# Kernel tuning notes

Measured on AMD Instinct MI355X. Metric: run time of the kernel, lower is better.

Reference implementation:

```python
import jax, jax.numpy as jnp
import numpy as np

GAMMA = 0.99

def _get_D(gamma, T, dtype=jnp.float32):
    # D[n, m] = gamma**(n-m) if n >= m else 0 (NaN/inf cleanup as in torch source)
    n = jnp.arange(T)
    diff = n[:, None] - n[None, :]
    return jnp.where(diff >= 0, jnp.power(jnp.asarray(gamma, dtype), jnp.maximum(diff, 0).astype(dtype)), jnp.zeros((), dtype))

def setup_inputs() -> dict:
    key = jax.random.key(0)
    kX, kQ, kK, kV = jax.random.split(key, 4)
    B, T, I, C = 2, 4096, 1024, 1024
    X = jax.random.normal(kX, (B, T, I), dtype=jnp.float32)
    att_mask = jnp.ones((B, T), dtype=jnp.float32)
    S_n = jnp.zeros((B, C, C), dtype=jnp.float32)
    # params initialized as randn/I per the torch module
    W_Q = jax.random.normal(kQ, (I, C), dtype=jnp.float32) / I
    W_K = jax.random.normal(kK, (I, C), dtype=jnp.float32) / I
    W_V = jax.random.normal(kV, (I, I), dtype=jnp.float32) / I
    return {"X": X, "att_mask": att_mask, "S_n": S_n, "W_Q": W_Q, "W_K": W_K, "W_V": W_V}

def reference(X, att_mask, S_n, W_Q, W_K, W_V):
    # COINBlock.forward_parallel (dropout in eval mode = identity; att_mask unused)
    B, T, _ = X.shape
    C = W_Q.shape[1]
    Q = X @ W_Q            # [B,T,C]
    K = X @ W_K            # [B,T,C]
    V = X @ W_V            # [B,T,I]
    A = jnp.einsum('btc,bsc->bts', Q, K)          # [B,T,T]
    A = A * _get_D(GAMMA, T, X.dtype)[None, :, :]  # decay-masked scores
    out = A @ V                                    # [B,T,I]
    out = jnp.swapaxes(out, -2, -1).reshape(B, T, C)  # faithful transpose+view (I == C)
    return out, S_n
```

## Files before the change

kernel.cpp:

```cpp
#include <hip/hip_runtime.h>
#include <cstdint>
#include <cstddef>


using bf16x8 = __attribute__((ext_vector_type(8))) short;
using s16x4  = __attribute__((ext_vector_type(4))) short;
using f32x4  = __attribute__((ext_vector_type(4))) float;

#define T_SEQ 4096
#define C_DIM 1024

static constexpr float L2G = -0.0144995697f;

__device__ __forceinline__ short f2bf(float f) {
  unsigned u = __builtin_bit_cast(unsigned, f);
  u += 0x7FFFu + ((u >> 16) & 1u);
  return (short)(u >> 16);
}

__device__ __forceinline__ void async_ld16(const short* g, const short* l) {
  __builtin_amdgcn_global_load_lds(
      (const __attribute__((address_space(1))) unsigned int*)(uintptr_t)g,
      (__attribute__((address_space(3))) unsigned int*)(unsigned)(uintptr_t)l,
      16, 0, 0);
}

#define FENCE asm volatile("" ::: "memory")
#define BAR   do { FENCE; __builtin_amdgcn_s_barrier(); FENCE; } while (0)
#define VMC(N) asm volatile("s_waitcnt vmcnt(" #N ")" ::: "memory")


__device__ __forceinline__ void gemm4p2(
    const short* __restrict__ A, const short* __restrict__ B,
    int lda, int ldb, int NT,
    short* __restrict__ lsA, short* __restrict__ lsB,
    f32x4 (&acc)[4][4])
{
  const int tid  = threadIdx.x;
  const int lane = tid & 63;
  const int wave = tid >> 6;
  const int wM   = wave >> 1;
  const int wN   = wave & 1;
  const int quad = lane >> 4;
  const int l15  = lane & 15;
  const int key  = l15 & 7;
  const int uk0  = (quad ^ key) * 8;
  const int uk1  = ((4 ^ quad) ^ key) * 8;
  const short* aR0 = lsA + (wM * 64 + l15) * 64 + uk0;
  const short* aR1 = lsA + (wM * 64 + l15) * 64 + uk1;
  const short* bR0 = lsB + (wN * 64 + l15) * 64 + uk0;
  const short* bR1 = lsB + (wN * 64 + l15) * 64 + uk1;
  const int rl0 = lane >> 3;
  const int cu  = ((lane & 7) ^ rl0) * 8;
  const short* pa[2][2];
  const short* pb[2][2];
#pragma unroll
  for (int u = 0; u < 2; ++u)
#pragma unroll
    for (int j = 0; j < 2; ++j) {
      pa[u][j] = A + (size_t)(u * 64 + (wave + 4 * j) * 8 + rl0) * lda + cu;
      pb[u][j] = B + (size_t)(u * 64 + (wave + 4 * j) * 8 + rl0) * ldb + cu;
    }

#define S4A(SLOT, TT)                                                               \
  { _Pragma("unroll")                                                               \
    for (int u = 0; u < 2; ++u)                                                     \
      _Pragma("unroll")                                                             \
      for (int j = 0; j < 2; ++j)                                                   \
        async_ld16(pa[u][j] + (size_t)(TT) * 64,                                    \
                   lsA + (SLOT) * 8192 + u * 4096 + (wave + 4 * j) * 512 + lane * 8); }
#define S4B(SLOT, TT)                                                               \
  { _Pragma("unroll")                                                               \
    for (int u = 0; u < 2; ++u)                                                     \
      _Pragma("unroll")                                                             \
      for (int j = 0; j < 2; ++j)                                                   \
        async_ld16(pb[u][j] + (size_t)(TT) * 64,                                    \
                   lsB + (SLOT) * 8192 + u * 4096 + (wave + 4 * j) * 512 + lane * 8); }

  bf16x8 afA[4][2], afB[4][2], b01A[2][2], b01B[2][2], b23[2][2];

#define RD_AF(DST, SLOT)                                                            \
  { _Pragma("unroll")                                                               \
    for (int i = 0; i < 4; ++i) {                                                   \
      DST[i][0] = *(const bf16x8*)(aR0 + (SLOT) * 8192 + i * 1024);                 \
      DST[i][1] = *(const bf16x8*)(aR1 + (SLOT) * 8192 + i * 1024);                 \
    } }
#define RD_B01(DST, SLOT)                                                           \
  { _Pragma("unroll")                                                               \
    for (int n = 0; n < 2; ++n) {                                                   \
      DST[n][0] = *(const bf16x8*)(bR0 + (SLOT) * 8192 + n * 1024);                 \
      DST[n][1] = *(const bf16x8*)(bR1 + (SLOT) * 8192 + n * 1024);                 \
    } }
#define RD_B23(SLOT)                                                                \
  { _Pragma("unroll")                                                               \
    for (int n = 0; n < 2; ++n) {                                                   \
      b23[n][0] = *(const bf16x8*)(bR0 + (SLOT) * 8192 + (2 + n) * 1024);           \
      b23[n][1] = *(const bf16x8*)(bR1 + (SLOT) * 8192 + (2 + n) * 1024);           \
    } }
#define MFLO(AF, B01)                                                               \
  { __builtin_amdgcn_s_setprio(1);                                                  \
    _Pragma("unroll")                                                               \
    for (int kk = 0; kk < 2; ++kk)                                                  \
      _Pragma("unroll")                                                             \
      for (int i = 0; i < 4; ++i)                                                   \
        _Pragma("unroll")                                                           \
        for (int n = 0; n < 2; ++n)                                                 \
          acc[i][n] = __builtin_amdgcn_mfma_f32_16x16x32_bf16(                      \
              AF[i][kk], B01[n][kk], acc[i][n], 0, 0, 0);                           \
    __builtin_amdgcn_s_setprio(0); }
#define MFHI(AF)                                                                    \
  { __builtin_amdgcn_s_setprio(1);                                                  \
    _Pragma("unroll")                                                               \
    for (int kk = 0; kk < 2; ++kk)                                                  \
      _Pragma("unroll")                                                             \
      for (int i = 0; i < 4; ++i)                                                   \
        _Pragma("unroll")                                                           \
        for (int n = 0; n < 2; ++n)                                                 \
          acc[i][2 + n] = __builtin_amdgcn_mfma_f32_16x16x32_bf16(                  \
              AF[i][kk], b23[n][kk], acc[i][2 + n], 0, 0, 0);                       \
    __builtin_amdgcn_s_setprio(0); }

  S4A(0, 0); S4B(0, 0); S4A(1, 1); S4B(1, 1);
  VMC(8);
  BAR;
  RD_AF(afA, 0);
  RD_B01(b01A, 0);

  int s0 = 0;
  for (int tp = 0; tp < NT; tp += 2) {
    int s1 = s0 + 1; if (s1 == 3) s1 = 0;
    int s2 = s1 + 1; if (s2 == 3) s2 = 0;
    const int s3 = s0;
    const bool g2 = (tp + 2 < NT);
    const bool g3 = (tp + 3 < NT);

    RD_B23(s0);
    if (g2) S4B(s2, tp + 2);
    MFLO(afA, b01A);
    if (g2) VMC(4); else VMC(0);
    BAR;
    RD_AF(afB, 1);
    RD_B01(b01B, s1);
    if (g2) S4A(0, tp + 2);
    MFHI(afA);
    if (g2) VMC(4); else VMC(0);
    BAR;
    RD_B23(s1);
    if (g3) S4B(s3, tp + 3);
    MFLO(afB, b01B);
    if (g3) VMC(4); else VMC(0);
    BAR;
    if (g2) { RD_AF(afA, 0); RD_B01(b01A, s2); }
    if (g3) S4A(1, tp + 3);
    MFHI(afB);
    if (g3) VMC(4); else VMC(0);
    BAR;

    s0 = s2;
  }
#undef S4A
#undef S4B
#undef RD_AF
#undef RD_B01
#undef RD_B23
#undef MFLO
#undef MFHI
}

__device__ __forceinline__ void gemm4p3(
    const short* __restrict__ A, const short* __restrict__ B,
    int lda, int ldb, int NT,
    short* __restrict__ lsA, short* __restrict__ lsB,
    f32x4 (&acc)[4][4])
{
  const int tid  = threadIdx.x;
  const int lane = tid & 63;
  const int wave = tid >> 6;
  const int wM   = wave >> 1;
  const int wN   = wave & 1;
  const int quad = lane >> 4;
  const int l15  = lane & 15;
  const int key  = l15 & 7;
  const int uk0  = (quad ^ key) * 8;
  const int uk1  = ((4 ^ quad) ^ key) * 8;
  const short* aR0 = lsA + (wM * 64 + l15) * 64 + uk0;
  const short* aR1 = lsA + (wM * 64 + l15) * 64 + uk1;
  const short* bR0 = lsB + (wN * 64 + l15) * 64 + uk0;
  const short* bR1 = lsB + (wN * 64 + l15) * 64 + uk1;
  const int rl0 = lane >> 3;
  const int cu  = ((lane & 7) ^ rl0) * 8;
  const short* pa[2][2];
  const short* pb[2][2];
#pragma unroll
  for (int u = 0; u < 2; ++u)
#pragma unroll
    for (int j = 0; j < 2; ++j) {
      pa[u][j] = A + (size_t)(u * 64 + (wave + 4 * j) * 8 + rl0) * lda + cu;
      pb[u][j] = B + (size_t)(u * 64 + (wave + 4 * j) * 8 + rl0) * ldb + cu;
    }

#define S4A(SLOT, TT)                                                               \
  { _Pragma("unroll")                                                               \
    for (int u = 0; u < 2; ++u)                                                     \
      _Pragma("unroll")                                                             \
      for (int j = 0; j < 2; ++j)                                                   \
        async_ld16(pa[u][j] + (size_t)(TT) * 64,                                    \
                   lsA + (SLOT) * 8192 + u * 4096 + (wave + 4 * j) * 512 + lane * 8); }
#define S4B(SLOT, TT)                                                               \
  { _Pragma("unroll")                                                               \
    for (int u = 0; u < 2; ++u)                                                     \
      _Pragma("unroll")                                                             \
      for (int j = 0; j < 2; ++j)                                                   \
        async_ld16(pb[u][j] + (size_t)(TT) * 64,                                    \
                   lsB + (SLOT) * 8192 + u * 4096 + (wave + 4 * j) * 512 + lane * 8); }

  bf16x8 afA[4][2], afB[4][2], b01A[2][2], b01B[2][2], b23[2][2];

#define RD_AF(DST, SLOT)                                                            \
  { _Pragma("unroll")                                                               \
    for (int i = 0; i < 4; ++i) {                                                   \
      DST[i][0] = *(const bf16x8*)(aR0 + (SLOT) * 8192 + i * 1024);                 \
      DST[i][1] = *(const bf16x8*)(aR1 + (SLOT) * 8192 + i * 1024);                 \
    } }
#define RD_B01(DST, SLOT)                                                           \
  { _Pragma("unroll")                                                               \
    for (int n = 0; n < 2; ++n) {                                                   \
      DST[n][0] = *(const bf16x8*)(bR0 + (SLOT) * 8192 + n * 1024);                 \
      DST[n][1] = *(const bf16x8*)(bR1 + (SLOT) * 8192 + n * 1024);                 \
    } }
#define RD_B23(SLOT)                                                                \
  { _Pragma("unroll")                                                               \
    for (int n = 0; n < 2; ++n) {                                                   \
      b23[n][0] = *(const bf16x8*)(bR0 + (SLOT) * 8192 + (2 + n) * 1024);           \
      b23[n][1] = *(const bf16x8*)(bR1 + (SLOT) * 8192 + (2 + n) * 1024);           \
    } }
#define MFLO(AF, B01)                                                               \
  { __builtin_amdgcn_s_setprio(1);                                                  \
    _Pragma("unroll")                                                               \
    for (int kk = 0; kk < 2; ++kk)                                                  \
      _Pragma("unroll")                                                             \
      for (int i = 0; i < 4; ++i)                                                   \
        _Pragma("unroll")                                                           \
        for (int n = 0; n < 2; ++n)                                                 \
          acc[i][n] = __builtin_amdgcn_mfma_f32_16x16x32_bf16(                      \
              AF[i][kk], B01[n][kk], acc[i][n], 0, 0, 0);                           \
    __builtin_amdgcn_s_setprio(0); }
#define MFHI(AF)                                                                    \
  { __builtin_amdgcn_s_setprio(1);                                                  \
    _Pragma("unroll")                                                               \
    for (int kk = 0; kk < 2; ++kk)                                                  \
      _Pragma("unroll")                                                             \
      for (int i = 0; i < 4; ++i)                                                   \
        _Pragma("unroll")                                                           \
        for (int n = 0; n < 2; ++n)                                                 \
          acc[i][2 + n] = __builtin_amdgcn_mfma_f32_16x16x32_bf16(                  \
              AF[i][kk], b23[n][kk], acc[i][2 + n], 0, 0, 0);                       \
    __builtin_amdgcn_s_setprio(0); }

  S4A(0, 0); S4B(0, 0); S4A(1, 1); S4B(1, 1);
  VMC(8);
  BAR;
  RD_AF(afA, 0);
  RD_B01(b01A, 0);

  int s0 = 0;
  for (int tp = 0; tp < NT; tp += 2) {
    int s1 = s0 + 1; if (s1 == 3) s1 = 0;
    int s2 = s1 + 1; if (s2 == 3) s2 = 0;
    const int s3 = s0;
    const bool g2 = (tp + 2 < NT);
    const bool g3 = (tp + 3 < NT);

    RD_B23(s0);
    if (g2) S4A(s2, tp + 2);
    MFLO(afA, b01A);
    if (g2) VMC(4); else VMC(0);
    BAR;
    RD_AF(afB, s1);
    RD_B01(b01B, s1);
    if (g2) S4B(s2, tp + 2);
    MFHI(afA);
    if (g2) VMC(4); else VMC(0);
    BAR;
    RD_B23(s1);
    if (g3) S4A(s3, tp + 3);
    MFLO(afB, b01B);
    if (g3) VMC(4); else VMC(0);
    BAR;
    if (g2) { RD_AF(afA, s2); RD_B01(b01A, s2); }
    if (g3) S4B(s3, tp + 3);
    MFHI(afB);
    if (g3) VMC(4); else VMC(0);
    BAR;

    s0 = s2;
  }
#undef S4A
#undef S4B
#undef RD_AF
#undef RD_B01
#undef RD_B23
#undef MFLO
#undef MFHI
}


__global__ __launch_bounds__(256) void k_convX(const float* __restrict__ x,
                                               short* __restrict__ y) {
  const size_t i = ((size_t)blockIdx.x * 256 + threadIdx.x) * 4;
  const float4 v = *(const float4*)(x + i);
  s16x4 o;
  o[0] = f2bf(v.x); o[1] = f2bf(v.y); o[2] = f2bf(v.z); o[3] = f2bf(v.w);
  *(s16x4*)(y + i) = o;
}

__global__ __launch_bounds__(256) void k_convWt(const float* __restrict__ Wq,
                                                const float* __restrict__ Wk,
                                                const float* __restrict__ Wv,
                                                short* __restrict__ Wtq,
                                                short* __restrict__ Wtk,
                                                short* __restrict__ Wtv) {
  const float* W = (blockIdx.z == 0) ? Wq : (blockIdx.z == 1) ? Wk : Wv;
  short* Wt      = (blockIdx.z == 0) ? Wtq : (blockIdx.z == 1) ? Wtk : Wtv;
  __shared__ float t[32][33];
  const int tx = threadIdx.x & 31;
  const int ty = threadIdx.x >> 5;
  const int bc = blockIdx.x * 32;
  const int bi = blockIdx.y * 32;
#pragma unroll
  for (int j = 0; j < 32; j += 8)
    t[ty + j][tx] = W[(size_t)(bi + ty + j) * 1024 + bc + tx];
  __syncthreads();
#pragma unroll
  for (int j = 0; j < 32; j += 8)
    Wt[(size_t)(bc + ty + j) * 1024 + bi + tx] = f2bf(t[tx][ty + j]);
}


__global__ __launch_bounds__(256, 2) void k_proj(
    const short* __restrict__ Xb, const short* __restrict__ Wtq,
    const short* __restrict__ Wtk, const short* __restrict__ Wtv,
    short* __restrict__ Qb, short* __restrict__ Kb, short* __restrict__ Vt) {
  __shared__ short lsA[2 * 8192];
  __shared__ short lsB[3 * 8192];
  f32x4 acc[4][4];
#pragma unroll
  for (int i = 0; i < 4; ++i)
#pragma unroll
    for (int j = 0; j < 4; ++j) acc[i][j] = 0.f;

  const int z  = blockIdx.y;
  const int bx = blockIdx.x;
  const short* Ab;
  const short* Bb;
  int m, n;
  if (z < 2) {
    m = bx >> 3; n = bx & 7;
    Ab = Xb + (size_t)m * 128 * 1024;
    Bb = (z ? Wtk : Wtq) + (size_t)n * 128 * 1024;
  } else {
    m = bx >> 6; n = bx & 63;
    Ab = Wtv + (size_t)m * 128 * 1024;
    Bb = Xb + (size_t)n * 128 * 1024;
  }
  gemm4p2(Ab, Bb, 1024, 1024, 16, lsA, lsB, acc);

  const int lane = threadIdx.x & 63, wave = threadIdx.x >> 6;
  const int wM = wave >> 1, wN = wave & 1;
  const int quad = lane >> 4, l15 = lane & 15;
  if (z < 2) {
    short* O = z ? Kb : Qb;
#pragma unroll
    for (int mi = 0; mi < 4; ++mi)
#pragma unroll
      for (int ni = 0; ni < 4; ++ni)
#pragma unroll
        for (int r = 0; r < 4; ++r) {
          const int row = m * 128 + wM * 64 + mi * 16 + quad * 4 + r;
          const int col = n * 128 + wN * 64 + ni * 16 + l15;
          O[(size_t)row * 1024 + col] = f2bf(acc[mi][ni][r]);
        }
  } else {
#pragma unroll
    for (int mi = 0; mi < 4; ++mi)
#pragma unroll
      for (int ni = 0; ni < 4; ++ni)
#pragma unroll
        for (int r = 0; r < 4; ++r) {
          const int crow = m * 128 + wM * 64 + mi * 16 + quad * 4 + r;
          const int t8   = n * 128 + wN * 64 + ni * 16 + l15;
          const int b = t8 >> 12, tt = t8 & 4095;
          Vt[(size_t)b * C_DIM * T_SEQ + (size_t)crow * T_SEQ + tt] =
              f2bf(acc[mi][ni][r]);
        }
  }
}

__global__ __launch_bounds__(256, 2) void k_scores(const short* __restrict__ Qb,
                                                   const short* __restrict__ Kb,
                                                   short* __restrict__ P) {
  __shared__ short lsA[2 * 8192];
  __shared__ short lsB[3 * 8192];
  f32x4 acc[4][4];
#pragma unroll
  for (int i = 0; i < 4; ++i)
#pragma unroll
    for (int j = 0; j < 4; ++j) acc[i][j] = 0.f;

  int id = blockIdx.x, mm = 0;
  while (id >= 32 - mm) { id -= 32 - mm; ++mm; }
  const int nn = mm + id;

  const size_t b = blockIdx.y;
  const short* Ab = Qb + b * T_SEQ * C_DIM + (size_t)nn * 128 * 1024;
  const short* Bb = Kb + b * T_SEQ * C_DIM + (size_t)mm * 128 * 1024;
  gemm4p2(Ab, Bb, 1024, 1024, 16, lsA, lsB, acc);

  short* Pb = P + b * (size_t)T_SEQ * T_SEQ;
  const int lane = threadIdx.x & 63, wave = threadIdx.x >> 6;
  const int wM = wave >> 1, wN = wave & 1;
  const int quad = lane >> 4, l15 = lane & 15;
#pragma unroll
  for (int mi = 0; mi < 4; ++mi)
#pragma unroll
    for (int ni = 0; ni < 4; ++ni)
#pragma unroll
      for (int r = 0; r < 4; ++r) {
        const int n = nn * 128 + wM * 64 + mi * 16 + quad * 4 + r;
        const int m = mm * 128 + wN * 64 + ni * 16 + l15;
        float v = 0.f;
        if (n >= m) v = acc[mi][ni][r] * exp2f((float)(n - m) * L2G);
        Pb[(size_t)n * T_SEQ + m] = f2bf(v);
      }
}

__global__ __launch_bounds__(256, 1) void k_pv(const short* __restrict__ Vt,
                                               const short* __restrict__ P,
                                               float* __restrict__ out) {
  __shared__ short lsA[3 * 8192];
  __shared__ short lsB[3 * 8192];
  const int p  = blockIdx.x;
  const int iy = blockIdx.y;
  const size_t b = blockIdx.z;

  const short* Ab = Vt + b * (size_t)C_DIM * T_SEQ + (size_t)iy * 128 * T_SEQ;
  const short* Pb = P + b * (size_t)T_SEQ * T_SEQ;
  float* Ob = out + b * (size_t)C_DIM * T_SEQ;

  const int lane = threadIdx.x & 63, wave = threadIdx.x >> 6;
  const int wM = wave >> 1, wN = wave & 1;
  const int quad = lane >> 4, l15 = lane & 15;

  const int cols[2] = { 31 - p, p };
#pragma unroll
  for (int cc = 0; cc < 2; ++cc) {
    const int c = cols[cc];
    f32x4 acc[4][4];
#pragma unroll
    for (int i = 0; i < 4; ++i)
#pragma unroll
      for (int j = 0; j < 4; ++j) acc[i][j] = 0.f;
    gemm4p3(Ab, Pb + (size_t)c * 128 * T_SEQ, T_SEQ, T_SEQ, 2 * c + 2,
            lsA, lsB, acc);
#pragma unroll
    for (int mi = 0; mi < 4; ++mi)
#pragma unroll
      for (int ni = 0; ni < 4; ++ni)
#pragma unroll
        for (int r = 0; r < 4; ++r) {
          const int irow = iy * 128 + wM * 64 + mi * 16 + quad * 4 + r;
          const int tcol = c * 128 + wN * 64 + ni * 16 + l15;
          Ob[(size_t)irow * T_SEQ + tcol] = acc[mi][ni][r];
        }
  }
}


extern "C" void kernel_launch(void* const* d_in, const int* in_sizes, int n_in,
                              void* d_out, int out_size, void* d_ws, size_t ws_size,
                              hipStream_t stream) {
  const float* X  = (const float*)d_in[0];
  const float* Wq = (const float*)d_in[3];
  const float* Wk = (const float*)d_in[4];
  const float* Wv = (const float*)d_in[5];
  float* out = (float*)d_out;

  char* ws = (char*)d_ws;
  short* Xb  = (short*)(ws);
  short* Wtq = (short*)(ws + 16777216);
  short* Wtk = (short*)(ws + 18874368);
  short* Wtv = (short*)(ws + 20971520);
  short* Qb  = (short*)(ws + 23068672);
  short* Kb  = (short*)(ws + 39845888);
  short* Vt  = (short*)(ws + 56623104);
  short* P   = (short*)(ws + 73400320);

  const size_t mainN = (size_t)2 * T_SEQ * C_DIM;
  hipMemsetAsync((char*)d_out + mainN * 4, 0,
                 ((size_t)out_size - mainN) * 4, stream);

  k_convX  <<<dim3(8192),       dim3(256), 0, stream>>>(X, Xb);
  k_convWt <<<dim3(32, 32, 3),  dim3(256), 0, stream>>>(Wq, Wk, Wv, Wtq, Wtk, Wtv);
  k_proj   <<<dim3(512, 3),     dim3(256), 0, stream>>>(Xb, Wtq, Wtk, Wtv, Qb, Kb, Vt);
  k_scores <<<dim3(528, 2),     dim3(256), 0, stream>>>(Qb, Kb, P);
  k_pv     <<<dim3(16, 8, 2),   dim3(256), 0, stream>>>(Vt, P, out);
}
```

Before: 269.3 us.

## Use 256x256 tiles with 8-wave GEMM for scores and remap blocks across XCDs

Adds a new 512-thread GEMM routine that computes 256x256 output tiles with double-buffered LDS, and uses it for the causal score kernel, cutting the tile count from 528 to 136 per batch. All three GEMM kernels switch to a 1D grid with a block-id swizzle that groups consecutive work onto the same XCD, aiming at better L2 reuse. Larger tiles raise data reuse per block but give coarser triangular granularity (more masked wasted work on the diagonal) and only 272 blocks, which may leave CUs idle or imbalanced.

```diff
diff --git a/kernel.cpp b/kernel.cpp
--- a/kernel.cpp
+++ b/kernel.cpp
@@ -29,6 +29,127 @@
 #define BAR   do { FENCE; __builtin_amdgcn_s_barrier(); FENCE; } while (0)
 #define VMC(N) asm volatile("s_waitcnt vmcnt(" #N ")" ::: "memory")
 
+
+__device__ __forceinline__ void gemm8p(
+    const short* __restrict__ A, const short* __restrict__ B,
+    int lda, int ldb, int NT,
+    short* __restrict__ lsA, short* __restrict__ lsB,
+    f32x4 (&acc)[8][4])
+{
+  const int tid  = threadIdx.x;
+  const int lane = tid & 63;
+  const int wave = tid >> 6;
+  const int wM   = wave >> 2;
+  const int wN   = wave & 3;
+  const int quad = lane >> 4;
+  const int l15  = lane & 15;
+  const int key  = l15 & 7;
+  const int uk0  = (quad ^ key) * 8;
+  const int uk1  = ((4 ^ quad) ^ key) * 8;
+  const short* aB0 = lsA + wM * 8192 + l15 * 64 + uk0;
+  const short* aB1 = lsA + wM * 8192 + l15 * 64 + uk1;
+  const short* bB0 = lsB + wN * 4096 + l15 * 64 + uk0;
+  const short* bB1 = lsB + wN * 4096 + l15 * 64 + uk1;
+  const int rl0 = lane >> 3;
+  const int cu  = ((lane & 7) ^ rl0) * 8;
+  const short* pa[4];
+  const short* pb[4];
+#pragma unroll
+  for (int j = 0; j < 4; ++j) {
+    const int grow = (wave * 4 + j) * 8 + rl0;
+    pa[j] = A + (size_t)grow * lda + cu;
+    pb[j] = B + (size_t)grow * ldb + cu;
+  }
+
+#define ST_A8(SLOT, TT)                                                             \
+  { _Pragma("unroll")                                                               \
+    for (int j = 0; j < 4; ++j)                                                     \
+      async_ld16(pa[j] + (size_t)(TT) * 64,                                         \
+                 lsA + (SLOT) * 16384 + (wave * 4 + j) * 512 + lane * 8); }
+#define ST_B8(SLOT, TT)                                                             \
+  { _Pragma("unroll")                                                               \
+    for (int j = 0; j < 4; ++j)                                                     \
+      async_ld16(pb[j] + (size_t)(TT) * 64,                                         \
+                 lsB + (SLOT) * 16384 + (wave * 4 + j) * 512 + lane * 8); }
+
+  bf16x8 af03k0[4], af03k1[4], af47k0[4], af47k1[4], bfk0[4], bfk1[4];
+
+  ST_A8(0, 0);
+  ST_B8(0, 0);
+  ST_B8(1, 1);
+  VMC(4);
+  BAR;
+#pragma unroll
+  for (int mi = 0; mi < 4; ++mi) af03k0[mi] = *(const bf16x8*)(aB0 + mi * 1024);
+#pragma unroll
+  for (int ni = 0; ni < 4; ++ni) bfk0[ni]   = *(const bf16x8*)(bB0 + ni * 1024);
+
+  for (int t = 0; t < NT; ++t) {
+    const int sA = (t & 1) * 16384;
+    const int sB = (t & 1) * 16384;
+
+#pragma unroll
+    for (int mi = 0; mi < 4; ++mi) af03k1[mi] = *(const bf16x8*)(aB1 + sA + mi * 1024);
+#pragma unroll
+    for (int ni = 0; ni < 4; ++ni) bfk1[ni]   = *(const bf16x8*)(bB1 + sB + ni * 1024);
+    if (t + 1 < NT) ST_A8((t + 1) & 1, t + 1);
+    __builtin_amdgcn_s_setprio(1);
+#pragma unroll
+    for (int mi = 0; mi < 4; ++mi)
+#pragma unroll
+      for (int ni = 0; ni < 4; ++ni)
+        acc[mi][ni] = __builtin_amdgcn_mfma_f32_16x16x32_bf16(
+            af03k0[mi], bfk0[ni], acc[mi][ni], 0, 0, 0);
+    __builtin_amdgcn_s_setprio(0);
+    BAR;
+
+#pragma unroll
+    for (int mi = 0; mi < 4; ++mi) af47k0[mi] = *(const bf16x8*)(aB0 + sA + 4096 + mi * 1024);
+    __builtin_amdgcn_s_setprio(1);
+#pragma unroll
+    for (int mi = 0; mi < 4; ++mi)
+#pragma unroll
+      for (int ni = 0; ni < 4; ++ni)
+        acc[mi][ni] = __builtin_amdgcn_mfma_f32_16x16x32_bf16(
+            af03k1[mi], bfk1[ni], acc[mi][ni], 0, 0, 0);
+    __builtin_amdgcn_s_setprio(0);
+    BAR;
+
+#pragma unroll
+    for (int mi = 0; mi < 4; ++mi) af47k1[mi] = *(const bf16x8*)(aB1 + sA + 4096 + mi * 1024);
+    if (t + 2 < NT) ST_B8(t & 1, t + 2);
+    __builtin_amdgcn_s_setprio(1);
+#pragma unroll
+    for (int mi = 0; mi < 4; ++mi)
+#pragma unroll
+      for (int ni = 0; ni < 4; ++ni)
+        acc[4 + mi][ni] = __builtin_amdgcn_mfma_f32_16x16x32_bf16(
+            af47k0[mi], bfk0[ni], acc[4 + mi][ni], 0, 0, 0);
+    __builtin_amdgcn_s_setprio(0);
+    if (t + 2 < NT) VMC(4); else VMC(0);
+    BAR;
+
+    if (t + 1 < NT) {
+      const int sA2 = ((t + 1) & 1) * 16384;
+      const int sB2 = ((t + 1) & 1) * 16384;
+#pragma unroll
+      for (int mi = 0; mi < 4; ++mi) af03k0[mi] = *(const bf16x8*)(aB0 + sA2 + mi * 1024);
+#pragma unroll
+      for (int ni = 0; ni < 4; ++ni) bfk0[ni]   = *(const bf16x8*)(bB0 + sB2 + ni * 1024);
+    }
+    __builtin_amdgcn_s_setprio(1);
+#pragma unroll
+    for (int mi = 0; mi < 4; ++mi)
+#pragma unroll
+      for (int ni = 0; ni < 4; ++ni)
+        acc[4 + mi][ni] = __builtin_amdgcn_mfma_f32_16x16x32_bf16(
+            af47k1[mi], bfk1[ni], acc[4 + mi][ni], 0, 0, 0);
+    __builtin_amdgcn_s_setprio(0);
+    BAR;
+  }
+#undef ST_A8
+#undef ST_B8
+}
 
 __device__ __forceinline__ void gemm4p2(
     const short* __restrict__ A, const short* __restrict__ B,
@@ -349,8 +470,10 @@
 #pragma unroll
     for (int j = 0; j < 4; ++j) acc[i][j] = 0.f;
 
-  const int z  = blockIdx.y;
-  const int bx = blockIdx.x;
+  const int bid = blockIdx.x;
+  const int wg  = (bid & 7) * 192 + (bid >> 3);
+  const int z   = wg / 512;
+  const int bx  = wg % 512;
   const short* Ab;
   const short* Bb;
   int m, n;
@@ -396,38 +519,40 @@
   }
 }
 
-__global__ __launch_bounds__(256, 2) void k_scores(const short* __restrict__ Qb,
+__global__ __launch_bounds__(512, 1) void k_scores(const short* __restrict__ Qb,
                                                    const short* __restrict__ Kb,
                                                    short* __restrict__ P) {
-  __shared__ short lsA[2 * 8192];
-  __shared__ short lsB[3 * 8192];
-  f32x4 acc[4][4];
-#pragma unroll
-  for (int i = 0; i < 4; ++i)
+  __shared__ short lsA[2 * 16384];
+  __shared__ short lsB[2 * 16384];
+  f32x4 acc[8][4];
+#pragma unroll
+  for (int i = 0; i < 8; ++i)
 #pragma unroll
     for (int j = 0; j < 4; ++j) acc[i][j] = 0.f;
 
-  int id = blockIdx.x, mm = 0;
-  while (id >= 32 - mm) { id -= 32 - mm; ++mm; }
+  const int bid = blockIdx.x;
+  const int wg  = (bid & 7) * 34 + (bid >> 3);
+  const size_t b = wg / 136;
+  int id = wg % 136, mm = 0;
+  while (id >= 16 - mm) { id -= 16 - mm; ++mm; }
   const int nn = mm + id;
 
-  const size_t b = blockIdx.y;
-  const short* Ab = Qb + b * T_SEQ * C_DIM + (size_t)nn * 128 * 1024;
-  const short* Bb = Kb + b * T_SEQ * C_DIM + (size_t)mm * 128 * 1024;
-  gemm4p2(Ab, Bb, 1024, 1024, 16, lsA, lsB, acc);
+  const short* Ab = Qb + b * T_SEQ * C_DIM + (size_t)nn * 256 * 1024;
+  const short* Bb = Kb + b * T_SEQ * C_DIM + (size_t)mm * 256 * 1024;
+  gemm8p(Ab, Bb, 1024, 1024, 16, lsA, lsB, acc);
 
   short* Pb = P + b * (size_t)T_SEQ * T_SEQ;
   const int lane = threadIdx.x & 63, wave = threadIdx.x >> 6;
-  const int wM = wave >> 1, wN = wave & 1;
+  const int wM = wave >> 2, wN = wave & 3;
   const int quad = lane >> 4, l15 = lane & 15;
 #pragma unroll
-  for (int mi = 0; mi < 4; ++mi)
+  for (int mi = 0; mi < 8; ++mi)
 #pragma unroll
     for (int ni = 0; ni < 4; ++ni)
 #pragma unroll
       for (int r = 0; r < 4; ++r) {
-        const int n = nn * 128 + wM * 64 + mi * 16 + quad * 4 + r;
-        const int m = mm * 128 + wN * 64 + ni * 16 + l15;
+        const int n = nn * 256 + wM * 128 + mi * 16 + quad * 4 + r;
+        const int m = mm * 256 + wN * 64 + ni * 16 + l15;
         float v = 0.f;
         if (n >= m) v = acc[mi][ni][r] * exp2f((float)(n - m) * L2G);
         Pb[(size_t)n * T_SEQ + m] = f2bf(v);
@@ -439,9 +564,12 @@
                                                float* __restrict__ out) {
   __shared__ short lsA[3 * 8192];
   __shared__ short lsB[3 * 8192];
-  const int p  = blockIdx.x;
-  const int iy = blockIdx.y;
-  const size_t b = blockIdx.z;
+  const int bid = blockIdx.x;
+  const int wg  = (bid & 7) * 32 + (bid >> 3);
+  const size_t b = wg >> 7;
+  const int r7   = wg & 127;
+  const int p    = r7 >> 3;
+  const int iy   = r7 & 7;
 
   const short* Ab = Vt + b * (size_t)C_DIM * T_SEQ + (size_t)iy * 128 * T_SEQ;
   const short* Pb = P + b * (size_t)T_SEQ * T_SEQ;
@@ -501,7 +629,7 @@
 
   k_convX  <<<dim3(8192),       dim3(256), 0, stream>>>(X, Xb);
   k_convWt <<<dim3(32, 32, 3),  dim3(256), 0, stream>>>(Wq, Wk, Wv, Wtq, Wtk, Wtv);
-  k_proj   <<<dim3(512, 3),     dim3(256), 0, stream>>>(Xb, Wtq, Wtk, Wtv, Qb, Kb, Vt);
-  k_scores <<<dim3(528, 2),     dim3(256), 0, stream>>>(Qb, Kb, P);
-  k_pv     <<<dim3(16, 8, 2),   dim3(256), 0, stream>>>(Vt, P, out);
-}
+  k_proj   <<<dim3(1536),       dim3(256), 0, stream>>>(Xb, Wtq, Wtk, Wtv, Qb, Kb, Vt);
+  k_scores <<<dim3(272),        dim3(512), 0, stream>>>(Qb, Kb, P);
+  k_pv     <<<dim3(256),        dim3(256), 0, stream>>>(Vt, P, out);
+}
```

New measurement: 278.0 us. 1.03x slower.
